# Kernel tuning notes

Measured on AMD Instinct MI355X. Metric: run time of the kernel, lower is better.

Reference implementation:

```python
import jax, jax.numpy as jnp
import numpy as np

N = 100000      # num_nodes
E = 1600000     # num_edges
D_IN = 256      # input_dim
H = 64          # hidden_dim
OUT = 32        # output_dim
EMB = 128       # node2vec embedding_dim
HEADS = 2       # GAT heads (concat=False -> mean over heads)
NEG_SLOPE = 0.2 # GATConv leaky_relu default


def setup_inputs() -> dict:
    key = jax.random.key(0)
    ks = jax.random.split(key, 24)
    s = lambda k, shape, fan: (jax.random.normal(k, shape, jnp.float32) * (1.0 / np.sqrt(fan)))
    return {
        "x": jax.random.normal(ks[0], (N, D_IN), jnp.float32),
        "edge_index": jax.random.randint(ks[1], (2, E), 0, N, jnp.int64),
        # frozen node2vec embedding table (used under no_grad in the original)
        "n2v_emb": jax.random.normal(ks[2], (N, EMB), jnp.float32),
        "n2v_proj_w": s(ks[3], (EMB, H), EMB), "n2v_proj_b": jnp.zeros((H,), jnp.float32),
        "input_proj_w": s(ks[4], (D_IN + H, H), D_IN + H), "input_proj_b": jnp.zeros((H,), jnp.float32),
        "gate_w": s(ks[5], (D_IN + H, H), D_IN + H), "gate_b": jnp.zeros((H,), jnp.float32),
        # SAGEConv layers: out = mean_agg(x_j) @ wl + bl + x @ wr
        "sage0_wl": s(ks[6], (H, H), H), "sage0_bl": jnp.zeros((H,), jnp.float32), "sage0_wr": s(ks[7], (H, H), H),
        "sage1_wl": s(ks[8], (H, H), H), "sage1_bl": jnp.zeros((H,), jnp.float32), "sage1_wr": s(ks[9], (H, H), H),
        # GATConv(H, H, heads=2, concat=False)
        "gat_w": s(ks[10], (H, HEADS * H), H),
        "gat_att_src": s(ks[11], (HEADS, H), H), "gat_att_dst": s(ks[12], (HEADS, H), H),
        "gat_b": jnp.zeros((H,), jnp.float32),
        "fin_wl": s(ks[13], (H, OUT), H), "fin_bl": jnp.zeros((OUT,), jnp.float32), "fin_wr": s(ks[14], (H, OUT), H),
    }


def _sage(h, src, dst, wl, bl, wr, n):
    # PyG SAGEConv with mean aggregation: lin_l(mean_j h_j) + lin_r(h_i)
    msum = jax.ops.segment_sum(h[src], dst, num_segments=n)
    deg = jax.ops.segment_sum(jnp.ones((src.shape[0],), h.dtype), dst, num_segments=n)
    agg = msum / jnp.maximum(deg, 1.0)[:, None]
    return agg @ wl + bl + h @ wr


def _gat(h, src, dst, w, att_src, att_dst, b, n):
    # GATConv with self-loops (PyG default), heads averaged (concat=False)
    loops = jnp.arange(n, dtype=src.dtype)
    src = jnp.concatenate([src, loops]); dst = jnp.concatenate([dst, loops])
    xh = (h @ w).reshape(n, HEADS, H)                     # [n, heads, H]
    a_src = jnp.einsum('nhd,hd->nh', xh, att_src)         # [n, heads]
    a_dst = jnp.einsum('nhd,hd->nh', xh, att_dst)
    e = jax.nn.leaky_relu(a_src[src] + a_dst[dst], NEG_SLOPE)  # [E', heads]
    emax = jax.ops.segment_max(e, dst, num_segments=n)
    ex = jnp.exp(e - emax[dst])
    esum = jax.ops.segment_sum(ex, dst, num_segments=n)
    alpha = ex / (esum[dst] + 1e-16)                      # edge softmax per dst, per head
    out = jax.ops.segment_sum(alpha[:, :, None] * xh[src], dst, num_segments=n)
    return out.mean(axis=1) + b                           # [n, H]


def reference(x, edge_index, n2v_emb, n2v_proj_w, n2v_proj_b, input_proj_w, input_proj_b,
              gate_w, gate_b, sage0_wl, sage0_bl, sage0_wr, sage1_wl, sage1_bl, sage1_wr,
              gat_w, gat_att_src, gat_att_dst, gat_b, fin_wl, fin_bl, fin_wr):
    n = x.shape[0]
    src, dst = edge_index[0], edge_index[1]
    # node2vec embeddings are frozen (torch.no_grad in original)
    n2v = jax.lax.stop_gradient(n2v_emb)
    n2v_p = n2v @ n2v_proj_w + n2v_proj_b                 # [n, H]
    combined = jnp.concatenate([x, n2v_p], axis=-1)       # [n, D_IN+H]
    gate = jax.nn.sigmoid(combined @ gate_w + gate_b)
    x_proj = combined @ input_proj_w + input_proj_b
    raw_proj = jnp.concatenate([x, jnp.zeros((n, H), x.dtype)], axis=-1) @ input_proj_w + input_proj_b
    h = gate * x_proj + (1.0 - gate) * raw_proj           # node_indices=None -> all nodes
    h = jax.nn.relu(_sage(h, src, dst, sage0_wl, sage0_bl, sage0_wr, n))
    h = jax.nn.relu(_sage(h, src, dst, sage1_wl, sage1_bl, sage1_wr, n))
    h = jax.nn.relu(_gat(h, src, dst, gat_w, gat_att_src, gat_att_dst, gat_b, n))
    return _sage(h, src, dst, fin_wl, fin_bl, fin_wr, n)  # [n, OUT]
```

## Files before the change

### kernel.cpp

```cpp
#include <hip/hip_runtime.h>
#include <math.h>

#define NN 100000
#define NE 1600000
#define DIN 256
#define HD 64
#define OUTD 32
#define EMBD 128
#define SLOPE 0.2f
#define AST 68
#define NT ((NN + 63) / 64)
#define SCHUNK 1024
#define SNBLK ((NN + SCHUNK - 1) / SCHUNK)

typedef __attribute__((ext_vector_type(8))) short bf16x8;
typedef __attribute__((ext_vector_type(8))) unsigned short u16x8;
typedef __attribute__((ext_vector_type(4))) float f32x4;

__device__ __forceinline__ float lrelu(float x) { return x > 0.f ? x : SLOPE * x; }
__device__ __forceinline__ ushort f2b(float f) {
    unsigned u = __float_as_uint(f);
    return (ushort)((u + 0x7FFFu + ((u >> 16) & 1u)) >> 16);
}
__device__ __forceinline__ float b2f(ushort v) { return __uint_as_float(((unsigned)v) << 16); }

__global__ void k_count(const int* __restrict__ dst, int* __restrict__ cnt) {
    int i = blockIdx.x * blockDim.x + threadIdx.x;
    if (i < NE) atomicAdd(&cnt[dst[i]], 1);
}

__global__ __launch_bounds__(256) void k_scan1(const int* __restrict__ cnt,
                                               int* __restrict__ rowptr,
                                               int* __restrict__ blksum) {
    __shared__ int ts[256];
    int base = blockIdx.x * SCHUNK + threadIdx.x * 4;
    int v0 = 0, v1 = 0, v2 = 0, v3 = 0;
    if (base < NN)     v0 = cnt[base];
    if (base + 1 < NN) v1 = cnt[base + 1];
    if (base + 2 < NN) v2 = cnt[base + 2];
    if (base + 3 < NN) v3 = cnt[base + 3];
    int s = v0 + v1 + v2 + v3;
    ts[threadIdx.x] = s;
    __syncthreads();
    for (int off = 1; off < 256; off <<= 1) {
        int w = (threadIdx.x >= off) ? ts[threadIdx.x - off] : 0;
        __syncthreads();
        ts[threadIdx.x] += w;
        __syncthreads();
    }
    int excl = ts[threadIdx.x] - s;
    if (base < NN)     rowptr[base]     = excl;
    if (base + 1 < NN) rowptr[base + 1] = excl + v0;
    if (base + 2 < NN) rowptr[base + 2] = excl + v0 + v1;
    if (base + 3 < NN) rowptr[base + 3] = excl + v0 + v1 + v2;
    if (threadIdx.x == 255) blksum[blockIdx.x] = ts[255];
}

__global__ __launch_bounds__(128) void k_scan2(int* __restrict__ blksum) {
    __shared__ int ts[128];
    int t = threadIdx.x;
    int v = (t < SNBLK) ? blksum[t] : 0;
    ts[t] = v;
    __syncthreads();
    for (int off = 1; off < 128; off <<= 1) {
        int w = (t >= off) ? ts[t - off] : 0;
        __syncthreads();
        ts[t] += w;
        __syncthreads();
    }
    if (t < SNBLK) blksum[t] = ts[t] - v;
}

__global__ void k_scan3(const int* __restrict__ blksum, const int* __restrict__ cnt,
                        int* __restrict__ rowptr, int* __restrict__ cursor,
                        float* __restrict__ invdeg) {
    int i = blockIdx.x * blockDim.x + threadIdx.x;
    if (i < NN) {
        int v = rowptr[i] + blksum[i >> 10];
        rowptr[i] = v;
        cursor[i] = v;
        invdeg[i] = 1.0f / fmaxf((float)cnt[i], 1.0f);
    }
    if (i == 0) rowptr[NN] = NE;
}

__global__ void k_fill(const int* __restrict__ src, const int* __restrict__ dst,
                       int* __restrict__ cursor, int* __restrict__ colsrc) {
    int i = blockIdx.x * blockDim.x + threadIdx.x;
    if (i >= NE) return;
    int pos = atomicAdd(&cursor[dst[i]], 1);
    colsrc[pos] = src[i];
}

__device__ __forceinline__ void stageA(const float* __restrict__ g, int nbase, int ldg, int koff,
                                       float (*As)[AST]) {
    for (int i = threadIdx.x; i < 1024; i += 256) {
        int m = i >> 4, k4 = (i & 15) << 2;
        int row = nbase + m;
        if (row >= NN) row = NN - 1;
        *(float4*)&As[m][k4] = *(const float4*)&g[(size_t)row * ldg + koff + k4];
    }
}
__device__ __forceinline__ void stageW(const float* __restrict__ g, float* Ws) {
    for (int i = threadIdx.x; i < 1024; i += 256) ((float4*)Ws)[i] = ((const float4*)g)[i];
}
__device__ __forceinline__ void stageWcols(const float* __restrict__ g, int ldg, int coff,
                                           float* Ws) {
    for (int i = threadIdx.x; i < 1024; i += 256) {
        int r = i >> 4, c4 = (i & 15) << 2;
        *(float4*)&Ws[r * 64 + c4] = *(const float4*)&g[r * ldg + coff + c4];
    }
}
__device__ __forceinline__ void mac16v(const float (*As)[AST], const float* __restrict__ Ws,
                                       float (*acc)[4], int tr, int tc) {
#pragma unroll 4
    for (int k4 = 0; k4 < 64; k4 += 4) {
        float4 a0 = *(const float4*)&As[tr * 4 + 0][k4];
        float4 a1 = *(const float4*)&As[tr * 4 + 1][k4];
        float4 a2 = *(const float4*)&As[tr * 4 + 2][k4];
        float4 a3 = *(const float4*)&As[tr * 4 + 3][k4];
#pragma unroll
        for (int j = 0; j < 4; j++) {
            float4 w = *(const float4*)&Ws[(k4 + j) * 64 + tc * 4];
            float e0 = (&a0.x)[j], e1 = (&a1.x)[j], e2 = (&a2.x)[j], e3 = (&a3.x)[j];
            acc[0][0] += e0 * w.x; acc[0][1] += e0 * w.y; acc[0][2] += e0 * w.z; acc[0][3] += e0 * w.w;
            acc[1][0] += e1 * w.x; acc[1][1] += e1 * w.y; acc[1][2] += e1 * w.z; acc[1][3] += e1 * w.w;
            acc[2][0] += e2 * w.x; acc[2][1] += e2 * w.y; acc[2][2] += e2 * w.z; acc[2][3] += e2 * w.w;
            acc[3][0] += e3 * w.x; acc[3][1] += e3 * w.y; acc[3][2] += e3 * w.z; acc[3][3] += e3 * w.w;
        }
    }
}

__global__ __launch_bounds__(256) void k_n2vp_t(const float* __restrict__ n2v,
                                                const float* __restrict__ w,
                                                const float* __restrict__ b,
                                                float* __restrict__ n2vp) {
    __shared__ float As[64][AST];
    __shared__ float Ws[64 * 64];
    int nbase = blockIdx.x * 64;
    int tc = threadIdx.x & 15, tr = threadIdx.x >> 4;
    float acc[4][4] = {};
    for (int c = 0; c < 2; c++) {
        if (c) __syncthreads();
        stageA(n2v, nbase, EMBD, c * 64, As);
        stageW(w + c * 64 * 64, Ws);
        __syncthreads();
        mac16v(As, Ws, acc, tr, tc);
    }
    float b0 = b[tc * 4], b1 = b[tc * 4 + 1], b2 = b[tc * 4 + 2], b3 = b[tc * 4 + 3];
#pragma unroll
    for (int i = 0; i < 4; i++) {
        int row = nbase + tr * 4 + i;
        if (row < NN) {
            float4 o = {acc[i][0] + b0, acc[i][1] + b1, acc[i][2] + b2, acc[i][3] + b3};
            *(float4*)&n2vp[(size_t)row * HD + tc * 4] = o;
        }
    }
}

__global__ __launch_bounds__(256) void k_front_t(const float* __restrict__ x,
                                                 const float* __restrict__ n2vp,
                                                 const float* __restrict__ ip_w,
                                                 const float* __restrict__ ip_b,
                                                 const float* __restrict__ gate_w,
                                                 const float* __restrict__ gate_b,
                                                 float* __restrict__ h0,
                                                 ushort* __restrict__ h0b) {
    __shared__ ushort Ah[64][40], Al[64][40];
    __shared__ ushort Bih[64][40], Bil[64][40];
    __shared__ ushort Bgh[64][40], Bgl[64][40];
    int nbase = blockIdx.x * 64;
    int tid = threadIdx.x;
    int w = tid >> 6, l = tid & 63;
    int lr = l & 15, lg = l >> 4, lk = lg * 8;
    f32x4 zero = {0.f, 0.f, 0.f, 0.f};
    f32x4 araw[4], ag[4], adel[4];
#pragma unroll
    for (int t = 0; t < 4; t++) { araw[t] = zero; ag[t] = zero; adel[t] = zero; }

    int arow = tid >> 2, ak0 = (tid & 3) << 3;
    int garow = nbase + arow;
    if (garow >= NN) garow = NN - 1;

    for (int c = 0; c < 8; c++) {
        if (c) __syncthreads();
        {
            const float* src = &x[(size_t)garow * DIN + c * 32 + ak0];
            u16x8 th, tl;
#pragma unroll
            for (int u = 0; u < 8; u++) {
                float v = src[u];
                ushort h = f2b(v);
                th[u] = h;
                tl[u] = f2b(v - b2f(h));
            }
            *(u16x8*)&Ah[arow][ak0] = th;
            *(u16x8*)&Al[arow][ak0] = tl;
        }
        {
            const float* pi = &ip_w[(size_t)(c * 32 + w * 8) * 64 + l];
            const float* pg = &gate_w[(size_t)(c * 32 + w * 8) * 64 + l];
            u16x8 ih, il, gh, gl2;
#pragma unroll
            for (int u = 0; u < 8; u++) {
                float v = pi[u * 64];
                ushort h = f2b(v);
                ih[u] = h; il[u] = f2b(v - b2f(h));
                float g = pg[u * 64];
                ushort hg = f2b(g);
                gh[u] = hg; gl2[u] = f2b(g - b2f(hg));
            }
            *(u16x8*)&Bih[l][w * 8] = ih;
            *(u16x8*)&Bil[l][w * 8] = il;
            *(u16x8*)&Bgh[l][w * 8] = gh;
            *(u16x8*)&Bgl[l][w * 8] = gl2;
        }
        __syncthreads();
        bf16x8 ah = *(const bf16x8*)&Ah[w * 16 + lr][lk];
        bf16x8 al = *(const bf16x8*)&Al[w * 16 + lr][lk];
#pragma unroll
        for (int t = 0; t < 4; t++) {
            int col = t * 16 + lr;
            bf16x8 bih = *(const bf16x8*)&Bih[col][lk];
            bf16x8 bil = *(const bf16x8*)&Bil[col][lk];
            bf16x8 bgh = *(const bf16x8*)&Bgh[col][lk];
            bf16x8 bgl = *(const bf16x8*)&Bgl[col][lk];
            f32x4 r = araw[t];
            r = __builtin_amdgcn_mfma_f32_16x16x32_bf16(ah, bih, r, 0, 0, 0);
            r = __builtin_amdgcn_mfma_f32_16x16x32_bf16(ah, bil, r, 0, 0, 0);
            r = __builtin_amdgcn_mfma_f32_16x16x32_bf16(al, bih, r, 0, 0, 0);
            araw[t] = r;
            f32x4 g = ag[t];
            g = __builtin_amdgcn_mfma_f32_16x16x32_bf16(ah, bgh, g, 0, 0, 0);
            g = __builtin_amdgcn_mfma_f32_16x16x32_bf16(ah, bgl, g, 0, 0, 0);
            g = __builtin_amdgcn_mfma_f32_16x16x32_bf16(al, bgh, g, 0, 0, 0);
            ag[t] = g;
        }
    }
    for (int c = 0; c < 2; c++) {
        __syncthreads();
        {
            const float* src = &n2vp[(size_t)garow * HD + c * 32 + ak0];
            u16x8 th, tl;
#pragma unroll
            for (int u = 0; u < 8; u++) {
                float v = src[u];
                ushort h = f2b(v);
                th[u] = h;
                tl[u] = f2b(v - b2f(h));
            }
            *(u16x8*)&Ah[arow][ak0] = th;
            *(u16x8*)&Al[arow][ak0] = tl;
        }
        {
            const float* pi = &ip_w[(size_t)(DIN + c * 32 + w * 8) * 64 + l];
            const float* pg = &gate_w[(size_t)(DIN + c * 32 + w * 8) * 64 + l];
            u16x8 ih, il, gh, gl2;
#pragma unroll
            for (int u = 0; u < 8; u++) {
                float v = pi[u * 64];
                ushort h = f2b(v);
                ih[u] = h; il[u] = f2b(v - b2f(h));
                float g = pg[u * 64];
                ushort hg = f2b(g);
                gh[u] = hg; gl2[u] = f2b(g - b2f(hg));
            }
            *(u16x8*)&Bih[l][w * 8] = ih;
            *(u16x8*)&Bil[l][w * 8] = il;
            *(u16x8*)&Bgh[l][w * 8] = gh;
            *(u16x8*)&Bgl[l][w * 8] = gl2;
        }
        __syncthreads();
        bf16x8 ah = *(const bf16x8*)&Ah[w * 16 + lr][lk];
        bf16x8 al = *(const bf16x8*)&Al[w * 16 + lr][lk];
#pragma unroll
        for (int t = 0; t < 4; t++) {
            int col = t * 16 + lr;
            bf16x8 bih = *(const bf16x8*)&Bih[col][lk];
            bf16x8 bil = *(const bf16x8*)&Bil[col][lk];
            bf16x8 bgh = *(const bf16x8*)&Bgh[col][lk];
            bf16x8 bgl = *(const bf16x8*)&Bgl[col][lk];
            f32x4 r = adel[t];
            r = __builtin_amdgcn_mfma_f32_16x16x32_bf16(ah, bih, r, 0, 0, 0);
            r = __builtin_amdgcn_mfma_f32_16x16x32_bf16(ah, bil, r, 0, 0, 0);
            r = __builtin_amdgcn_mfma_f32_16x16x32_bf16(al, bih, r, 0, 0, 0);
            adel[t] = r;
            f32x4 g = ag[t];
            g = __builtin_amdgcn_mfma_f32_16x16x32_bf16(ah, bgh, g, 0, 0, 0);
            g = __builtin_amdgcn_mfma_f32_16x16x32_bf16(ah, bgl, g, 0, 0, 0);
            g = __builtin_amdgcn_mfma_f32_16x16x32_bf16(al, bgh, g, 0, 0, 0);
            ag[t] = g;
        }
    }
#pragma unroll
    for (int t = 0; t < 4; t++) {
        int col = t * 16 + lr;
        float ib = ip_b[col], gb2 = gate_b[col];
#pragma unroll
        for (int r = 0; r < 4; r++) {
            int row = nbase + w * 16 + lg * 4 + r;
            if (row < NN) {
                float raw = araw[t][r] + ib;
                float sg = 1.f / (1.f + __expf(-(ag[t][r] + gb2)));
                float o = raw + sg * adel[t][r];
                h0[(size_t)row * HD + col] = o;
                h0b[(size_t)row * HD + col] = f2b(o);
            }
        }
    }
}

__global__ void k_gather_mean(const int* __restrict__ rowptr, const int* __restrict__ colsrc,
                              const float* __restrict__ invdeg, const ushort* __restrict__ hb,
                              float* __restrict__ agg) {
    int t = threadIdx.x & 63;
    int lane = t & 31, half = t >> 5;
    int gw = blockIdx.x * (blockDim.x >> 6) + (threadIdx.x >> 6);
    int stride = gridDim.x * (blockDim.x >> 6);
    for (int n = gw; n < NN; n += stride) {
        int bg = rowptr[n], en = rowptr[n + 1];
        float a0 = 0.f, a1 = 0.f;
        int i = bg + half;
        for (; i + 6 < en; i += 8) {
            int sa = colsrc[i], sb = colsrc[i + 2], sc = colsrc[i + 4], sd = colsrc[i + 6];
            ushort2 va = *(const ushort2*)&hb[(size_t)sa * HD + lane * 2];
            ushort2 vb = *(const ushort2*)&hb[(size_t)sb * HD + lane * 2];
            ushort2 vc = *(const ushort2*)&hb[(size_t)sc * HD + lane * 2];
            ushort2 vd = *(const ushort2*)&hb[(size_t)sd * HD + lane * 2];
            a0 += b2f(va.x) + b2f(vb.x) + b2f(vc.x) + b2f(vd.x);
            a1 += b2f(va.y) + b2f(vb.y) + b2f(vc.y) + b2f(vd.y);
        }
        for (; i < en; i += 2) {
            int s = colsrc[i];
            ushort2 v = *(const ushort2*)&hb[(size_t)s * HD + lane * 2];
            a0 += b2f(v.x);
            a1 += b2f(v.y);
        }
        a0 += __shfl_xor(a0, 32);
        a1 += __shfl_xor(a1, 32);
        if (half == 0) {
            float id = invdeg[n];
            float2 o = {a0 * id, a1 * id};
            *(float2*)&agg[(size_t)n * HD + lane * 2] = o;
        }
    }
}

__global__ __launch_bounds__(256) void k_sage_t(const float* __restrict__ agg,
                                                const float* __restrict__ h,
                                                const float* __restrict__ wl,
                                                const float* __restrict__ bl,
                                                const float* __restrict__ wr,
                                                float* __restrict__ hout,
                                                ushort* __restrict__ houtb) {
    __shared__ float As[64][AST];
    __shared__ float Ws[64 * 64];
    int nbase = blockIdx.x * 64;
    int tc = threadIdx.x & 15, tr = threadIdx.x >> 4;
    float acc[4][4] = {};
    stageA(agg, nbase, HD, 0, As);
    stageW(wl, Ws);
    __syncthreads();
    mac16v(As, Ws, acc, tr, tc);
    __syncthreads();
    stageA(h, nbase, HD, 0, As);
    stageW(wr, Ws);
    __syncthreads();
    mac16v(As, Ws, acc, tr, tc);
    float b0 = bl[tc * 4], b1 = bl[tc * 4 + 1], b2 = bl[tc * 4 + 2], b3 = bl[tc * 4 + 3];
#pragma unroll
    for (int i = 0; i < 4; i++) {
        int row = nbase + tr * 4 + i;
        if (row < NN) {
            float4 o = {fmaxf(acc[i][0] + b0, 0.f), fmaxf(acc[i][1] + b1, 0.f),
                        fmaxf(acc[i][2] + b2, 0.f), fmaxf(acc[i][3] + b3, 0.f)};
            *(float4*)&hout[(size_t)row * HD + tc * 4] = o;
            ushort4 ob = {f2b(o.x), f2b(o.y), f2b(o.z), f2b(o.w)};
            *(ushort4*)&houtb[(size_t)row * HD + tc * 4] = ob;
        }
    }
}

__global__ __launch_bounds__(256) void k_gatxh_t(const float* __restrict__ h,
                                                 const float* __restrict__ w,
                                                 const float* __restrict__ att_s,
                                                 const float* __restrict__ att_d,
                                                 ushort* __restrict__ xhb,
                                                 float* __restrict__ a_s,
                                                 float* __restrict__ a_d) {
    __shared__ float As[64][AST];
    __shared__ float Ws[64 * 64];
    int nbase = blockIdx.x * 64;
    int tc = threadIdx.x & 15, tr = threadIdx.x >> 4;
    stageA(h, nbase, HD, 0, As);
#pragma unroll
    for (int half = 0; half < 2; half++) {
        if (half) __syncthreads();
        stageWcols(w, 128, half * 64, Ws);
        __syncthreads();
        float acc[4][4] = {};
        mac16v(As, Ws, acc, tr, tc);
        float as0 = att_s[half * 64 + tc * 4], as1 = att_s[half * 64 + tc * 4 + 1];
        float as2 = att_s[half * 64 + tc * 4 + 2], as3 = att_s[half * 64 + tc * 4 + 3];
        float ad0 = att_d[half * 64 + tc * 4], ad1 = att_d[half * 64 + tc * 4 + 1];
        float ad2 = att_d[half * 64 + tc * 4 + 2], ad3 = att_d[half * 64 + tc * 4 + 3];
#pragma unroll
        for (int i = 0; i < 4; i++) {
            int row = nbase + tr * 4 + i;
            float ps = acc[i][0] * as0 + acc[i][1] * as1 + acc[i][2] * as2 + acc[i][3] * as3;
            float pd = acc[i][0] * ad0 + acc[i][1] * ad1 + acc[i][2] * ad2 + acc[i][3] * ad3;
#pragma unroll
            for (int off = 8; off; off >>= 1) {
                ps += __shfl_xor(ps, off);
                pd += __shfl_xor(pd, off);
            }
            if (row < NN) {
                ushort4 ob = {f2b(acc[i][0]), f2b(acc[i][1]), f2b(acc[i][2]), f2b(acc[i][3])};
                *(ushort4*)&xhb[(size_t)row * 128 + half * 64 + tc * 4] = ob;
                if (tc == 0) {
                    a_s[row * 2 + half] = ps;
                    a_d[row * 2 + half] = pd;
                }
            }
        }
    }
}

__global__ void k_gat_fused(const int* __restrict__ rowptr, const int* __restrict__ colsrc,
                            const float* __restrict__ a_s, const float* __restrict__ a_d,
                            const ushort* __restrict__ xhb, const float* __restrict__ gb,
                            float* __restrict__ hout) {
    int t = threadIdx.x & 63;
    int lane = t & 31, half = t >> 5;
    int bl4 = (lane & 15) * 4;
    float4 bias4 = *(const float4*)&gb[bl4];
    int gw = blockIdx.x * (blockDim.x >> 6) + (threadIdx.x >> 6);
    int stride = gridDim.x * (blockDim.x >> 6);
    for (int n = gw; n < NN; n += stride) {
        int bg = rowptr[n], en = rowptr[n + 1];
        float ad0 = a_d[n * 2], ad1 = a_d[n * 2 + 1];
        float a0 = 0.f, a1 = 0.f, a2 = 0.f, a3 = 0.f;
        float ss0 = 0.f, ss1 = 0.f;
        int i = bg + half;
        for (; i + 2 < en; i += 4) {
            int sa = colsrc[i], sb = colsrc[i + 2];
            float2 ava = *(const float2*)&a_s[sa * 2];
            float2 avb = *(const float2*)&a_s[sb * 2];
            ushort4 xva = *(const ushort4*)&xhb[(size_t)sa * 128 + lane * 4];
            ushort4 xvb = *(const ushort4*)&xhb[(size_t)sb * 128 + lane * 4];
            float wa0 = __expf(lrelu(ava.x + ad0));
            float wa1 = __expf(lrelu(ava.y + ad1));
            float wb0 = __expf(lrelu(avb.x + ad0));
            float wb1 = __expf(lrelu(avb.y + ad1));
            ss0 += wa0 + wb0;
            ss1 += wa1 + wb1;
            float wsa = (lane < 16) ? wa0 : wa1;
            float wsb = (lane < 16) ? wb0 : wb1;
            a0 += wsa * b2f(xva.x) + wsb * b2f(xvb.x);
            a1 += wsa * b2f(xva.y) + wsb * b2f(xvb.y);
            a2 += wsa * b2f(xva.z) + wsb * b2f(xvb.z);
            a3 += wsa * b2f(xva.w) + wsb * b2f(xvb.w);
        }
        for (; i < en; i += 2) {
            int s = colsrc[i];
            float2 av = *(const float2*)&a_s[s * 2];
            float w0 = __expf(lrelu(av.x + ad0));
            float w1 = __expf(lrelu(av.y + ad1));
            ss0 += w0;
            ss1 += w1;
            float wsel = (lane < 16) ? w0 : w1;
            ushort4 xv = *(const ushort4*)&xhb[(size_t)s * 128 + lane * 4];
            a0 += wsel * b2f(xv.x);
            a1 += wsel * b2f(xv.y);
            a2 += wsel * b2f(xv.z);
            a3 += wsel * b2f(xv.w);
        }
        if (half == 0) {
            float2 av = *(const float2*)&a_s[n * 2];
            float w0 = __expf(lrelu(av.x + ad0));
            float w1 = __expf(lrelu(av.y + ad1));
            ss0 += w0;
            ss1 += w1;
            float wsel = (lane < 16) ? w0 : w1;
            ushort4 xv = *(const ushort4*)&xhb[(size_t)n * 128 + lane * 4];
            a0 += wsel * b2f(xv.x);
            a1 += wsel * b2f(xv.y);
            a2 += wsel * b2f(xv.z);
            a3 += wsel * b2f(xv.w);
        }
        ss0 += __shfl_xor(ss0, 32);
        ss1 += __shfl_xor(ss1, 32);
        a0 += __shfl_xor(a0, 32);
        a1 += __shfl_xor(a1, 32);
        a2 += __shfl_xor(a2, 32);
        a3 += __shfl_xor(a3, 32);
        float r = (lane < 16) ? (0.5f / (ss0 + 1e-16f)) : (0.5f / (ss1 + 1e-16f));
        float v0 = a0 * r, v1 = a1 * r, v2 = a2 * r, v3 = a3 * r;
        float p0 = __shfl_xor(v0, 16);
        float p1 = __shfl_xor(v1, 16);
        float p2 = __shfl_xor(v2, 16);
        float p3 = __shfl_xor(v3, 16);
        if (half == 0 && lane < 16) {
            float4 o = {fmaxf(v0 + p0 + bias4.x, 0.f), fmaxf(v1 + p1 + bias4.y, 0.f),
                        fmaxf(v2 + p2 + bias4.z, 0.f), fmaxf(v3 + p3 + bias4.w, 0.f)};
            *(float4*)&hout[(size_t)n * HD + lane * 4] = o;
        }
    }
}

__global__ void k_pfin(const float* __restrict__ h, const float* __restrict__ wl,
                       ushort* __restrict__ Pb) {
    __shared__ float sw[HD * OUTD];
    for (int i = threadIdx.x; i < HD * OUTD; i += blockDim.x) sw[i] = wl[i];
    __syncthreads();
    int t = threadIdx.x & 63;
    int c = t & 31, half = t >> 5;
    int gw = blockIdx.x * (blockDim.x >> 6) + (threadIdx.x >> 6);
    int stride = gridDim.x * (blockDim.x >> 6);
    for (int n = gw; n < NN; n += stride) {
        float hv = h[(size_t)n * HD + t];
        float acc = 0.f;
#pragma unroll 8
        for (int i = 0; i < 32; i++) {
            float bb = __shfl(hv, half * 32 + i);
            acc += bb * sw[half * 1024 + i * 32 + c];
        }
        acc += __shfl_xor(acc, 32);
        if (half == 0) Pb[(size_t)n * OUTD + c] = f2b(acc);
    }
}

__global__ void k_final_fused(const int* __restrict__ rowptr, const int* __restrict__ colsrc,
                              const float* __restrict__ invdeg, const ushort* __restrict__ Pb,
                              const float* __restrict__ h, const float* __restrict__ bl,
                              const float* __restrict__ wr, float* __restrict__ out) {
    __shared__ float sw[HD * OUTD];
    for (int i = threadIdx.x; i < HD * OUTD; i += blockDim.x) sw[i] = wr[i];
    __syncthreads();
    int t = threadIdx.x & 63;
    int j = t & 31, half = t >> 5;
    int quarter = t >> 4, lane16 = t & 15;
    float bias = bl[j];
    int gw = blockIdx.x * (blockDim.x >> 6) + (threadIdx.x >> 6);
    int stride = gridDim.x * (blockDim.x >> 6);
    for (int n = gw; n < NN; n += stride) {
        int bg = rowptr[n], en = rowptr[n + 1];
        float a0 = 0.f, a1 = 0.f;
        int i = bg + quarter;
        for (; i + 4 < en; i += 8) {
            int sa = colsrc[i], sb = colsrc[i + 4];
            ushort2 va = *(const ushort2*)&Pb[(size_t)sa * OUTD + lane16 * 2];
            ushort2 vb = *(const ushort2*)&Pb[(size_t)sb * OUTD + lane16 * 2];
            a0 += b2f(va.x) + b2f(vb.x);
            a1 += b2f(va.y) + b2f(vb.y);
        }
        for (; i < en; i += 4) {
            int s = colsrc[i];
            ushort2 v = *(const ushort2*)&Pb[(size_t)s * OUTD + lane16 * 2];
            a0 += b2f(v.x);
            a1 += b2f(v.y);
        }
        a0 += __shfl_xor(a0, 32);
        a1 += __shfl_xor(a1, 32);
        a0 += __shfl_xor(a0, 16);
        a1 += __shfl_xor(a1, 16);
        float hv = h[(size_t)n * HD + t];
        float o = 0.f;
#pragma unroll 8
        for (int i2 = 0; i2 < 32; i2++) {
            float bb = __shfl(hv, half * 32 + i2);
            o += bb * sw[half * 1024 + i2 * 32 + j];
        }
        o += __shfl_xor(o, 32);
        float ga = __shfl(a0, j >> 1);
        float gb_ = __shfl(a1, j >> 1);
        float gv = (j & 1) ? gb_ : ga;
        if (half == 0) out[(size_t)n * OUTD + j] = gv * invdeg[n] + bias + o;
    }
}

extern "C" void kernel_launch(void* const* d_in, const int* in_sizes, int n_in,
                              void* d_out, int out_size, void* d_ws, size_t ws_size,
                              hipStream_t stream) {
    const float* x      = (const float*)d_in[0];
    const int*   eidx   = (const int*)d_in[1];
    const float* n2v    = (const float*)d_in[2];
    const float* n2v_w  = (const float*)d_in[3];
    const float* n2v_b  = (const float*)d_in[4];
    const float* ip_w   = (const float*)d_in[5];
    const float* ip_b   = (const float*)d_in[6];
    const float* gate_w = (const float*)d_in[7];
    const float* gate_b = (const float*)d_in[8];
    const float* s0_wl  = (const float*)d_in[9];
    const float* s0_bl  = (const float*)d_in[10];
    const float* s0_wr  = (const float*)d_in[11];
    const float* s1_wl  = (const float*)d_in[12];
    const float* s1_bl  = (const float*)d_in[13];
    const float* s1_wr  = (const float*)d_in[14];
    const float* gat_w  = (const float*)d_in[15];
    const float* att_s  = (const float*)d_in[16];
    const float* att_d  = (const float*)d_in[17];
    const float* gat_b  = (const float*)d_in[18];
    const float* f_wl   = (const float*)d_in[19];
    const float* f_bl   = (const float*)d_in[20];
    const float* f_wr   = (const float*)d_in[21];

    const int* src = eidx;
    const int* dst = eidx + NE;

    float*  ws     = (float*)d_ws;
    float*  invdeg = ws;
    float*  S1     = invdeg + NN;
    float*  S2     = S1 + (size_t)NN * HD;
    float*  SA     = S2 + (size_t)NN * HD;
    float*  a_s    = SA + (size_t)NN * HD;
    float*  a_d    = a_s + (size_t)NN * 2;
    ushort* Pb     = (ushort*)(a_d + (size_t)NN * 2);
    ushort* hb     = Pb + (size_t)NN * OUTD;
    ushort* xhb    = hb + (size_t)NN * HD;
    int*    cnt    = (int*)(xhb + (size_t)NN * 128);
    int*    rowptr = cnt + NN;
    int*    cursor = rowptr + NN + 1;
    int*    blksum = cursor + NN;
    int*    colsrc = blksum + 128;

    float* n2vp = SA;
    float* agg  = SA;
    float* out  = (float*)d_out;

    const int BT = 256;
    dim3 b128(128), b256(BT);
    int eblk = (NE + BT - 1) / BT;
    int nblk = (NN + BT - 1) / BT;

    hipMemsetAsync(cnt, 0, (size_t)NN * 4, stream);
    k_count<<<eblk, b256, 0, stream>>>(dst, cnt);
    k_scan1<<<SNBLK, b256, 0, stream>>>(cnt, rowptr, blksum);
    k_scan2<<<1, b128, 0, stream>>>(blksum);
    k_scan3<<<nblk, b256, 0, stream>>>(blksum, cnt, rowptr, cursor, invdeg);
    k_fill<<<eblk, b256, 0, stream>>>(src, dst, cursor, colsrc);

    k_n2vp_t<<<NT, b256, 0, stream>>>(n2v, n2v_w, n2v_b, n2vp);
    k_front_t<<<NT, b256, 0, stream>>>(x, n2vp, ip_w, ip_b, gate_w, gate_b, S2, hb);

    k_gather_mean<<<2048, b256, 0, stream>>>(rowptr, colsrc, invdeg, hb, agg);
    k_sage_t<<<NT, b256, 0, stream>>>(agg, S2, s0_wl, s0_bl, s0_wr, S1, hb);

    k_gather_mean<<<2048, b256, 0, stream>>>(rowptr, colsrc, invdeg, hb, agg);
    k_sage_t<<<NT, b256, 0, stream>>>(agg, S1, s1_wl, s1_bl, s1_wr, S2, hb);

    k_gatxh_t<<<NT, b256, 0, stream>>>(S2, gat_w, att_s, att_d, xhb, a_s, a_d);
    k_gat_fused<<<2048, b256, 0, stream>>>(rowptr, colsrc, a_s, a_d, xhb, gat_b, S1);

    k_pfin<<<2048, b256, 0, stream>>>(S1, f_wl, Pb);
    k_final_fused<<<2048, b256, 0, stream>>>(rowptr, colsrc, invdeg, Pb, S1, f_bl, f_wr, out);
}
```

Measured before the change: 709.3 us.

## Split CSR fill into bucketed pass plus per-block LDS scatter

Replaces the single per-edge global atomic scatter into CSR with two passes. The first scatters (src,dst) pairs into buckets of 64 destination nodes using global atomics on bucket cursors. The second has one block per bucket place each edge into its final slot using LDS atomics. This is meant to localize the random writes and cut per-node global atomic traffic, at the cost of an extra pass over an 8-byte pair buffer that reuses the xhb region.

```diff
diff --git a/kernel.cpp b/kernel.cpp
--- a/kernel.cpp
+++ b/kernel.cpp
@@ -12,6 +12,7 @@
 #define NT ((NN + 63) / 64)
 #define SCHUNK 1024
 #define SNBLK ((NN + SCHUNK - 1) / SCHUNK)
+#define NB ((NN + 63) / 64)
 
 typedef __attribute__((ext_vector_type(8))) short bf16x8;
 typedef __attribute__((ext_vector_type(8))) unsigned short u16x8;
@@ -72,24 +73,46 @@
 }
 
 __global__ void k_scan3(const int* __restrict__ blksum, const int* __restrict__ cnt,
-                        int* __restrict__ rowptr, int* __restrict__ cursor,
+                        int* __restrict__ rowptr, int* __restrict__ bcursor,
                         float* __restrict__ invdeg) {
     int i = blockIdx.x * blockDim.x + threadIdx.x;
     if (i < NN) {
         int v = rowptr[i] + blksum[i >> 10];
         rowptr[i] = v;
-        cursor[i] = v;
+        if ((i & 63) == 0) bcursor[i >> 6] = v;
         invdeg[i] = 1.0f / fmaxf((float)cnt[i], 1.0f);
     }
     if (i == 0) rowptr[NN] = NE;
 }
 
-__global__ void k_fill(const int* __restrict__ src, const int* __restrict__ dst,
-                       int* __restrict__ cursor, int* __restrict__ colsrc) {
+__global__ void k_fillA(const int* __restrict__ src, const int* __restrict__ dst,
+                        int* __restrict__ bcursor, int2* __restrict__ pairbuf) {
     int i = blockIdx.x * blockDim.x + threadIdx.x;
     if (i >= NE) return;
-    int pos = atomicAdd(&cursor[dst[i]], 1);
-    colsrc[pos] = src[i];
+    int s = src[i], d = dst[i];
+    int pos = atomicAdd(&bcursor[d >> 6], 1);
+    pairbuf[pos] = make_int2(s, d);
+}
+
+__global__ __launch_bounds__(256) void k_fillB(const int* __restrict__ rowptr,
+                                               const int2* __restrict__ pairbuf,
+                                               int* __restrict__ colsrc) {
+    __shared__ int lcur[64];
+    int b = blockIdx.x;
+    int nb0 = b * 64;
+    int t = threadIdx.x;
+    if (t < 64) {
+        int node = nb0 + t;
+        lcur[t] = (node < NN) ? rowptr[node] : NE;
+    }
+    __syncthreads();
+    int start = rowptr[nb0];
+    int end = (nb0 + 64 <= NN) ? rowptr[nb0 + 64] : NE;
+    for (int i = start + t; i < end; i += 256) {
+        int2 p = pairbuf[i];
+        int pos = atomicAdd(&lcur[p.y & 63], 1);
+        colsrc[pos] = p.x;
+    }
 }
 
 __device__ __forceinline__ void stageA(const float* __restrict__ g, int nbase, int ldg, int koff,
@@ -620,9 +643,11 @@
     ushort* xhb    = hb + (size_t)NN * HD;
     int*    cnt    = (int*)(xhb + (size_t)NN * 128);
     int*    rowptr = cnt + NN;
-    int*    cursor = rowptr + NN + 1;
-    int*    blksum = cursor + NN;
+    int*    bcursor = rowptr + NN + 1;
+    int*    blksum = bcursor + NB;
     int*    colsrc = blksum + 128;
+
+    int2* pairbuf = (int2*)xhb;
 
     float* n2vp = SA;
     float* agg  = SA;
@@ -637,8 +662,9 @@
     k_count<<<eblk, b256, 0, stream>>>(dst, cnt);
     k_scan1<<<SNBLK, b256, 0, stream>>>(cnt, rowptr, blksum);
     k_scan2<<<1, b128, 0, stream>>>(blksum);
-    k_scan3<<<nblk, b256, 0, stream>>>(blksum, cnt, rowptr, cursor, invdeg);
-    k_fill<<<eblk, b256, 0, stream>>>(src, dst, cursor, colsrc);
+    k_scan3<<<nblk, b256, 0, stream>>>(blksum, cnt, rowptr, bcursor, invdeg);
+    k_fillA<<<eblk, b256, 0, stream>>>(src, dst, bcursor, pairbuf);
+    k_fillB<<<NB, b256, 0, stream>>>(rowptr, pairbuf, colsrc);
 
     k_n2vp_t<<<NT, b256, 0, stream>>>(n2v, n2v_w, n2v_b, n2vp);
     k_front_t<<<NT, b256, 0, stream>>>(x, n2vp, ip_w, ip_b, gate_w, gate_b, S2, hb);
```

New measurement: 838.5 us. 1.18x slower.
